# Performance work log

Hardware: AMD Instinct MI355X
Metric: run time of the kernel (lower is better)

Reference implementation:

```python
import jax, jax.numpy as jnp
import numpy as np

MIN_CONF = 0.1      # forward kwarg min_conf (also used as rasterize conf_thresh)
NMS_KS = 3
ITERS = 30
LAM = 0.8
LAMBDA_E = 2.0


def _resize_linear(x, out_size, axis):
    """1D linear resize along `axis` with align_corners=True semantics."""
    n = x.shape[axis]
    if out_size == n:
        return x
    if n == 1:
        reps = [1] * x.ndim
        reps[axis] = out_size
        return jnp.tile(x, reps)
    pos = jnp.arange(out_size, dtype=x.dtype) * ((n - 1) / (out_size - 1))
    lo = jnp.clip(jnp.floor(pos).astype(jnp.int32), 0, n - 1)
    hi = jnp.minimum(lo + 1, n - 1)
    w = pos - lo.astype(x.dtype)
    shp = [1] * x.ndim
    shp[axis] = out_size
    w = w.reshape(shp)
    xl = jnp.take(x, lo, axis=axis)
    xh = jnp.take(x, hi, axis=axis)
    return xl * (1.0 - w) + xh * w


def _interp3d_prob(P_lr, Dhr, H, W):
    """Trilinear (separable) upsample of [B,D,H4,W4] prob volume + renorm over D."""
    x = _resize_linear(P_lr, Dhr, 1)
    x = _resize_linear(x, H, 2)
    x = _resize_linear(x, W, 3)
    return x / (x.sum(1, keepdims=True) + 1e-6)


def _shift(x, dy, dx):
    """Replicate-padded spatial shift of [B,1,H,W] (matches torch _shift)."""
    H, W = x.shape[-2], x.shape[-1]
    p = jnp.pad(x, ((0, 0), (0, 0), (max(dy, 0), max(-dy, 0)), (max(dx, 0), max(-dx, 0))), mode='edge')
    return p[..., max(-dy, 0):H + max(-dy, 0), max(-dx, 0):W + max(-dx, 0)]


def _forward(P_lr, edge, occ, H, W, topk):
    B, Dlr, H4, W4 = P_lr.shape
    scale_x = float(W) / float(W4)
    Dhr = max(1, int(round(Dlr * scale_x)))

    # _fullres_prob is @torch.no_grad in the original -> stop_gradient
    P_full = jax.lax.stop_gradient(_interp3d_prob(P_lr, Dhr, H, W))  # [B,Dhr,H,W]

    d_vals = jnp.arange(Dhr, dtype=P_full.dtype)[None, :, None, None]
    disp_init = (P_full * d_vals).sum(1, keepdims=True)  # soft-argmin [B,1,H,W]

    # --- extract_sparse_anchors (dense, jit-friendly equivalent) ---
    pmax = P_full.max(1)                      # [B,H,W]
    d_hat = jnp.argmax(P_full, 1)             # [B,H,W]
    top2 = jax.lax.top_k(jnp.moveaxis(P_full, 1, -1), 2)[0]  # [B,H,W,2]
    p2 = top2[..., 1]
    psr = pmax / (p2 + 1e-6)
    conf = pmax * jnp.tanh(psr)
    conf = conf * jnp.exp(-2.0 * edge[:, 0]) * jnp.clip(1.0 - occ[:, 0], 0.0, None)

    # 2D NMS (ties kept): max_pool2d 3x3 stride 1, SAME padding with -inf
    pool = jax.lax.reduce_window(conf, -np.inf, jax.lax.max,
                                 (1, NMS_KS, NMS_KS), (1, 1, 1), 'SAME')
    keep = (conf >= MIN_CONF) & (conf >= pool)  # [B,H,W]

    # per-batch topk cap on anchors
    HW = H * W
    flat = jnp.where(keep, conf, -jnp.inf).reshape(B, HW)
    vals, idx = jax.lax.top_k(flat, topk)
    ok = vals > -jnp.inf
    def _scatter(i, v):
        return jnp.zeros((HW,), dtype=bool).at[i].set(v)
    keep_final = jax.vmap(_scatter)(idx, ok).reshape(B, H, W)[:, None]  # [B,1,H,W]

    # --- rasterize_dense_uspf ---
    d_map = jnp.where(keep_final, jnp.clip(d_hat, 0, Dhr - 1).astype(jnp.float32)[:, None], 0.0)
    c_map = jnp.where(keep_final, jnp.clip(conf, 0.0, 1.0)[:, None], 0.0)
    valid = keep_final & (c_map >= MIN_CONF)

    # --- refine_with_sparse_anchors_full: edge-aware diffusion of residual ---
    delta = jax.lax.stop_gradient(d_map - disp_init)
    m = jax.lax.stop_gradient(c_map * valid.astype(jnp.float32))

    e, o = edge, occ
    e_up, o_up = _shift(e, -1, 0), _shift(o, -1, 0)
    e_dn, o_dn = _shift(e, 1, 0), _shift(o, 1, 0)
    e_lf, o_lf = _shift(e, 0, -1), _shift(o, 0, -1)
    e_rt, o_rt = _shift(e, 0, 1), _shift(o, 0, 1)
    w_up = jnp.exp(-LAMBDA_E * (e + e_up) / 2) * (1 - o) * (1 - o_up)
    w_dn = jnp.exp(-LAMBDA_E * (e + e_dn) / 2) * (1 - o) * (1 - o_dn)
    w_lf = jnp.exp(-LAMBDA_E * (e + e_lf) / 2) * (1 - o) * (1 - o_lf)
    w_rt = jnp.exp(-LAMBDA_E * (e + e_rt) / 2) * (1 - o) * (1 - o_rt)
    w_sum = w_up + w_dn + w_lf + w_rt + 1e-6
    denom = m + LAM * w_sum + 1e-6
    num0 = m * delta

    def body(_, R):
        nbr = (w_up * _shift(R, -1, 0) + w_dn * _shift(R, 1, 0)
               + w_lf * _shift(R, 0, -1) + w_rt * _shift(R, 0, 1))
        return (num0 + LAM * nbr) / denom

    R = jax.lax.fori_loop(0, ITERS, body, jnp.zeros_like(disp_init))
    disp_full = jnp.clip(disp_init + R, 0.0, None)
    return disp_full


def setup_inputs() -> dict:
    key = jax.random.key(0)
    k1, k2, k3 = jax.random.split(key, 3)
    # spiky probability volume over D so that confident anchors exist
    P_lr = jax.nn.softmax(8.0 * jax.random.normal(k1, (1, 32, 96, 192), dtype=jnp.float32), axis=1)
    edge = 0.2 * jax.random.uniform(k2, (1, 1, 384, 768), dtype=jnp.float32)
    occ = 0.2 * jax.random.uniform(k3, (1, 1, 384, 768), dtype=jnp.float32)
    return {"P_lr": P_lr, "edge": edge, "occ": occ, "H": 384, "W": 768, "topk": 8000}


def reference(P_lr, edge, occ, H, W, topk):
    return _forward(P_lr, edge, occ, H, W, topk)
```

## Files before the change

### kernel.cpp

```cpp
#include <hip/hip_runtime.h>
#include <hip/hip_bf16.h>

typedef unsigned int u32;
typedef unsigned long long u64;

#define HH 384
#define WW 768
#define HW (HH*WW)
#define H4 96
#define W4 192
#define DLR 32
#define TOPK 8000
#define NTH 256
#define NBLK (HW/NTH)

#define PTW 18
#define PTH 3

#define JIW 48
#define JIH 32
#define JH  12
#define JRW 72
#define JRH 56
#define JNU (JRH*(JRW/4))
#define JGRID 192

#define KB16 0x3DCCu
#define NB16 448

struct SelState { u32 K, cutoff, idxcut; };

struct DTab {
    float A[32]; float B[32];
    int f[32]; int l[32];
    float w[128];
};
constexpr DTab mk_dtab(){
    DTab t{};
    const float CD = (float)(31.0/127.0);
    for (int k = 0; k < 32; ++k){ t.A[k]=0.f; t.B[k]=0.f; t.f[k]=-1; t.l[k]=-1; }
    for (int d = 0; d < 128; ++d){
        float pos = (float)d * CD;
        int lo = (int)pos; if (lo > 31) lo = 31;
        int hi = (lo+1 > 31) ? 31 : lo+1;
        float w = pos - (float)lo;
        t.w[d] = w;
        t.A[lo] += 1.0f - w;            t.A[hi] += w;
        t.B[lo] += (float)d*(1.0f - w); t.B[hi] += (float)d*w;
        if (t.f[lo] < 0) t.f[lo] = d;
        t.l[lo] = d;
    }
    return t;
}
static constexpr DTab DT = mk_dtab();

__global__ __launch_bounds__(NTH) void k_prob(const float* __restrict__ P,
        const float* __restrict__ edge, const float* __restrict__ occ,
        float* __restrict__ conf, float* __restrict__ disp0, u32* __restrict__ dhk,
        SelState* st){
    if (blockIdx.x == 0 && threadIdx.x == 0){
        st->K = 0; st->cutoff = 0; st->idxcut = 0x7FFFFFFFu;
    }

    __shared__ float Sl[DLR][PTH][PTW];
    __shared__ float YL[4][DLR][19];

    int bx = blockIdx.x % 12, by = blockIdx.x / 12;
    int X = bx*64, Y = by*4;
    const float CY = (float)(95.0/383.0);
    const float CX = (float)(191.0/767.0);

    float fy0 = (float)Y * CY; int y0min = (int)fy0; if (y0min > H4-1) y0min = H4-1;
    float fx0 = (float)X * CX; int x0min = (int)fx0; if (x0min > W4-1) x0min = W4-1;

    for (int e = threadIdx.x; e < DLR*PTH*PTW; e += NTH){
        int dl  = e / (PTH*PTW);
        int rem = e % (PTH*PTW);
        int ry  = rem / PTW;
        int cx  = rem % PTW;
        int gy = min(y0min + ry, H4-1);
        int gx = min(x0min + cx, W4-1);
        ((float*)Sl)[e] = P[dl*(H4*W4) + gy*W4 + gx];
    }
    __syncthreads();

    for (int e = threadIdx.x; e < 4*DLR*18; e += NTH){
        int ly  = e / (DLR*18);
        int rem = e % (DLR*18);
        int dl  = rem / 18;
        int cx  = rem % 18;
        float fy = (float)(Y + ly) * CY;
        int y0 = (int)fy; if (y0 > H4-1) y0 = H4-1;
        int y1 = min(y0+1, H4-1);
        float wy = fy - (float)y0;
        int ry = y0 - y0min, ryb = y1 - y0min;
        YL[ly][dl][cx] = Sl[dl][ry][cx]*(1.0f-wy) + Sl[dl][ryb][cx]*wy;
    }
    __syncthreads();

    int lx = threadIdx.x & 63, ly = threadIdx.x >> 6;
    int x = X + lx, y = Y + ly;
    int idx = y*WW + x;

    float fx = (float)x * CX;
    int x0 = (int)fx; if (x0 > W4-1) x0 = W4-1;
    float wx = fx - (float)x0;
    float omwx = 1.0f - wx;
    int cxl = x0 - x0min;

    float S[DLR];
    #pragma unroll
    for (int k = 0; k < DLR; ++k)
        S[k] = YL[ly][k][cxl]*omwx + YL[ly][k][cxl+1]*wx;

    float s0=0.f,s1=0.f,s2=0.f,s3=0.f, u0=0.f,u1=0.f,u2=0.f,u3=0.f;
    #pragma unroll
    for (int k = 0; k < DLR; k += 4){
        s0 = fmaf(DT.A[k  ], S[k  ], s0); u0 = fmaf(DT.B[k  ], S[k  ], u0);
        s1 = fmaf(DT.A[k+1], S[k+1], s1); u1 = fmaf(DT.B[k+1], S[k+1], u1);
        s2 = fmaf(DT.A[k+2], S[k+2], s2); u2 = fmaf(DT.B[k+2], S[k+2], u2);
        s3 = fmaf(DT.A[k+3], S[k+3], s3); u3 = fmaf(DT.B[k+3], S[k+3], u3);
    }
    float sum  = (s0+s1) + (s2+s3);
    float sumd = (u0+u1) + (u2+u3);

    float vmax = -1.f, v2 = -1.f; int dmax = 0;
    #pragma unroll
    for (int k = 0; k < 32; ++k){
        if (DT.f[k] < 0) continue;
        const int d0 = DT.f[k], d1 = DT.l[k];
        const int kh = (k+1 > 31) ? 31 : k+1;
        float Sk = S[k], Sh = S[kh];
        const float w0 = DT.w[d0], w1 = DT.w[d1];
        float vf = Sk*(1.0f-w0) + Sh*w0;
        float vl = Sk*(1.0f-w1) + Sh*w1;
        bool up = vl > vf;
        float segv = up ? vl : vf;
        int   segd = up ? d1 : d0;
        float vr = -1.f;
        if (d1 > d0){
            const float wa = DT.w[d1-1], wb = DT.w[d0+1];
            float va = Sk*(1.0f-wa) + Sh*wa;
            float vb = Sk*(1.0f-wb) + Sh*wb;
            vr = up ? va : vb;
        }
        if (segv > vmax){ v2 = fmaxf(vmax, vr); vmax = segv; dmax = segd; }
        else            { v2 = fmaxf(v2, segv); }
    }

    float inv  = 1.0f/(sum + 1e-6f);
    float pmax = vmax*inv, p2 = v2*inv;
    float psr  = pmax/(p2 + 1e-6f);
    float cf   = pmax * tanhf(psr);
    cf *= expf(-2.0f*edge[idx]) * fmaxf(1.0f - occ[idx], 0.0f);
    conf[idx]  = cf;
    disp0[idx] = sumd*inv;
    dhk[idx]   = (u32)dmax;
}

__global__ __launch_bounds__(NTH) void k_nms(const float* __restrict__ conf,
        const float* __restrict__ edge, const float* __restrict__ occ,
        u32* __restrict__ dhk, float4* __restrict__ w4raw,
        u64* __restrict__ list, SelState* st){
    __shared__ float Cs[6][66];
    __shared__ float Es[6][66];
    __shared__ float Os[6][66];
    int bx = blockIdx.x % 12, by = blockIdx.x / 12;
    int X = bx*64, Y = by*4;
    for (int e = threadIdx.x; e < 6*66; e += NTH){
        int ry = e / 66, cx = e % 66;
        int gy = Y + ry - 1, gx = X + cx - 1;
        bool in = ((u32)gy < (u32)HH) && ((u32)gx < (u32)WW);
        int cg = min(max(gy,0),HH-1)*WW + min(max(gx,0),WW-1);
        Cs[ry][cx] = in ? conf[cg] : -INFINITY;
        Es[ry][cx] = edge[cg];
        Os[ry][cx] = occ[cg];
    }
    __syncthreads();

    int lx = threadIdx.x & 63, ly = threadIdx.x >> 6;
    int x = X + lx, y = Y + ly;
    int idx = y*WW + x;

    float c = Cs[ly+1][lx+1];
    float pool = Cs[ly][lx];
    pool = fmaxf(pool, Cs[ly  ][lx+1]); pool = fmaxf(pool, Cs[ly  ][lx+2]);
    pool = fmaxf(pool, Cs[ly+1][lx  ]); pool = fmaxf(pool, Cs[ly+1][lx+1]);
    pool = fmaxf(pool, Cs[ly+1][lx+2]);
    pool = fmaxf(pool, Cs[ly+2][lx  ]); pool = fmaxf(pool, Cs[ly+2][lx+1]);
    pool = fmaxf(pool, Cs[ly+2][lx+2]);
    bool keep = (c >= 0.1f) && (c >= pool);
    dhk[idx] |= keep ? 256u : 0u;

    float e  = Es[ly+1][lx+1], o  = Os[ly+1][lx+1];
    float e1 = Es[ly+2][lx+1], o1 = Os[ly+2][lx+1];
    float e2 = Es[ly  ][lx+1], o2 = Os[ly  ][lx+1];
    float e3 = Es[ly+1][lx+2], o3 = Os[ly+1][lx+2];
    float e4 = Es[ly+1][lx  ], o4 = Os[ly+1][lx  ];
    float4 wp;
    wp.x = expf(-(e+e1))*(1.f-o)*(1.f-o1);
    wp.y = expf(-(e+e2))*(1.f-o)*(1.f-o2);
    wp.z = expf(-(e+e3))*(1.f-o)*(1.f-o3);
    wp.w = expf(-(e+e4))*(1.f-o)*(1.f-o4);
    w4raw[idx] = wp;

    u64 m = __ballot(keep);
    int lane = threadIdx.x & 63, wid = threadIdx.x >> 6;
    __shared__ u32 wc[4];
    __shared__ u32 wpre[4];
    __shared__ u32 bb;
    if (lane == 0) wc[wid] = (u32)__popcll(m);
    __syncthreads();
    if (threadIdx.x == 0){
        u32 s = 0;
        #pragma unroll
        for (int w = 0; w < 4; ++w){ wpre[w] = s; s += wc[w]; }
        bb = atomicAdd(&st->K, s);
    }
    __syncthreads();
    if (keep){
        u32 before = (u32)__popcll(m & ((1ull << lane) - 1ull));
        u32 pos = bb + wpre[wid] + before;
        list[pos] = ((u64)__float_as_uint(c) << 32) | (u32)idx;
    }
}

__global__ __launch_bounds__(1024) void k_sel(const u64* __restrict__ list,
        u64* __restrict__ side, SelState* st){
    u32 n = st->K;
    if (n <= TOPK) return;

    __shared__ u32 wh[16][NB16+1];
    __shared__ u32 hs[512];
    __shared__ u32 sc[512];
    __shared__ u32 hh[256];
    __shared__ u32 bc[3];
    __shared__ u32 snc;
    int t = threadIdx.x;
    int lane = t & 63, wv = t >> 6;

    for (int e = t; e < 16*(NB16+1); e += 1024) ((u32*)wh)[e] = 0;
    if (t == 0) snc = 0;
    __syncthreads();

    u32 nh = n >> 1;
    const ulonglong2* list2 = (const ulonglong2*)list;
    for (u32 p = t; p < nh; p += 1024){
        ulonglong2 e2 = list2[p];
        int b0 = (int)((u32)(e2.x >> 48)) - (int)KB16;
        int b1 = (int)((u32)(e2.y >> 48)) - (int)KB16;
        b0 = min(max(b0, 0), NB16-1);
        b1 = min(max(b1, 0), NB16-1);
        atomicAdd(&wh[wv][b0], 1u);
        atomicAdd(&wh[wv][b1], 1u);
    }
    if ((n & 1u) && t == 0){
        int b = (int)((u32)(list[n-1] >> 48)) - (int)KB16;
        b = min(max(b, 0), NB16-1);
        atomicAdd(&wh[0][b], 1u);
    }
    __syncthreads();
    if (t < 512){
        u32 s = 0;
        if (t < NB16){
            #pragma unroll
            for (int w = 0; w < 16; ++w) s += wh[w][t];
        }
        hs[t] = s;
    }
    __syncthreads();

    u32 rem = TOPK;
    if (t < 512) sc[t] = hs[511 - t];
    __syncthreads();
    for (int off = 1; off < 512; off <<= 1){
        u32 add = (t < 512 && t >= off) ? sc[t - off] : 0;
        __syncthreads();
        if (t < 512) sc[t] += add;
        __syncthreads();
    }
    if (t < 512){
        u32 Sd  = sc[511 - t];
        u32 Sd1 = (t == 511) ? 0u : sc[511 - (t+1)];
        if (Sd >= rem && Sd1 < rem){ bc[0] = (u32)t; bc[1] = rem - Sd1; }
    }
    __syncthreads();
    u32 p16 = KB16 + bc[0];
    rem = bc[1];
    __syncthreads();

    if (t < 256) hh[t] = 0;
    __syncthreads();
    u32 npad = (n + 1023u) & ~1023u;
    for (u32 i = t; i < npad; i += 1024){
        bool match = false; u64 e = 0; u32 key = 0;
        if (i < n){
            e = list[i];
            key = (u32)(e >> 32);
            match = (key >> 16) == p16;
        }
        u64 mb = __ballot(match);
        u32 cnt = (u32)__popcll(mb);
        if (cnt){
            int ldr = (int)(__ffsll((long long)mb) - 1);
            u32 base = 0;
            if (lane == ldr) base = atomicAdd(&snc, cnt);
            base = __shfl(base, ldr);
            if (match){
                u32 before = (u32)__popcll(mb & ((1ull << lane) - 1ull));
                side[base + before] = e;
                atomicAdd(&hh[(key >> 8) & 255u], 1u);
            }
        }
    }
    __syncthreads();
    u32 msz = snc;

    if (t < 256) sc[t] = hh[255 - t];
    __syncthreads();
    for (int off = 1; off < 256; off <<= 1){
        u32 add = (t < 256 && t >= off) ? sc[t - off] : 0;
        __syncthreads();
        if (t < 256) sc[t] += add;
        __syncthreads();
    }
    if (t < 256){
        u32 Sd  = sc[255 - t];
        u32 Sd1 = (t == 255) ? 0u : sc[255 - (t+1)];
        if (Sd >= rem && Sd1 < rem){ bc[0] = (u32)t; bc[1] = rem - Sd1; }
    }
    __syncthreads();
    u32 d1 = bc[0]; rem = bc[1];
    u32 pref24 = (p16 << 8) | d1;
    __syncthreads();

    if (t < 256) hh[t] = 0;
    __syncthreads();
    u32 mpad = (msz + 1023u) & ~1023u;
    for (u32 i = t; i < mpad; i += 1024){
        if (i < msz){
            u32 key = (u32)(side[i] >> 32);
            if ((key >> 8) == pref24) atomicAdd(&hh[key & 255u], 1u);
        }
    }
    __syncthreads();
    if (t < 256) sc[t] = hh[255 - t];
    __syncthreads();
    for (int off = 1; off < 256; off <<= 1){
        u32 add = (t < 256 && t >= off) ? sc[t - off] : 0;
        __syncthreads();
        if (t < 256) sc[t] += add;
        __syncthreads();
    }
    if (t < 256){
        u32 Sd  = sc[255 - t];
        u32 Sd1 = (t == 255) ? 0u : sc[255 - (t+1)];
        if (Sd >= rem && Sd1 < rem){ bc[0] = (u32)t; bc[1] = rem - Sd1; bc[2] = hh[t]; }
    }
    __syncthreads();
    u32 cutoff = (pref24 << 8) | bc[0];
    rem = bc[1];
    u32 tie_h = bc[2];
    __syncthreads();

    u32 idxcut = 0x7FFFFFFFu;
    if (rem != tie_h){
        u32 iprefix = 0, irem = rem;
        for (int b = 2; b >= 0; --b){
            if (t < 256) hh[t] = 0;
            __syncthreads();
            int shift = 8*b;
            for (u32 i = t; i < mpad; i += 1024){
                if (i < msz){
                    u64 e = side[i];
                    u32 key = (u32)(e >> 32);
                    u32 idx = (u32)e;
                    if (key == cutoff && (((u64)(idx ^ iprefix)) >> (shift+8)) == 0)
                        atomicAdd(&hh[(idx >> shift) & 255u], 1u);
                }
            }
            __syncthreads();
            if (t < 256) sc[t] = hh[t];
            __syncthreads();
            for (int off = 1; off < 256; off <<= 1){
                u32 add = (t < 256 && t >= off) ? sc[t - off] : 0;
                __syncthreads();
                if (t < 256) sc[t] += add;
                __syncthreads();
            }
            if (t < 256){
                u32 Pd = sc[t];
                u32 Pm = (t == 0) ? 0u : sc[t-1];
                if (Pd >= irem && Pm < irem){ bc[0] = (u32)t; bc[1] = irem - Pm; }
            }
            __syncthreads();
            iprefix |= bc[0] << shift; irem = bc[1];
            __syncthreads();
        }
        idxcut = iprefix;
    }
    if (t == 0){ st->cutoff = cutoff; st->idxcut = idxcut; }
}

template<int FUSED, int FINAL>
__global__ __launch_bounds__(NTH) void k_jacT(
        const float* __restrict__ Rin, float* __restrict__ Rout,
        const float4* __restrict__ Wp, const float* __restrict__ Nh,
        float4* __restrict__ Ws, float* __restrict__ Nho,
        const float* __restrict__ conf, const float* __restrict__ disp0,
        const u32* __restrict__ dhk, const SelState* __restrict__ st,
        float* __restrict__ out, int K){
    __shared__ float Rs[2][JRH*JRW];
    int tid = threadIdx.x;
    int bx = blockIdx.x & 15, by = blockIdx.x >> 4;
    int ry0 = by*JIH - JH, cx0 = bx*JIW - JH;

    float4 Wt[4][4];
    float4 Nt[4];
    float4 Ct[4];

    u32 cut = 0, idxcut = 0;
    if (FUSED){ cut = st->cutoff; idxcut = st->idxcut; }

    #pragma unroll
    for (int k = 0; k < 4; ++k){
        int u = tid + k*NTH;
        if (u < JNU){
            int r = u / 18, c = (u % 18) << 2;
            int gy = ry0 + r;
            int cgy = min(max(gy,0),HH-1);
            float4 n4, r4;
            #pragma unroll
            for (int j = 0; j < 4; ++j){
                int gx = cx0 + c + j;
                int cgx = min(max(gx,0),WW-1);
                int g = cgy*WW + cgx;
                if (FUSED){
                    u32 dv = dhk[g];
                    float cf = conf[g];
                    u32 key = __float_as_uint(cf);
                    bool kf = (dv & 256u) &&
                              (key > cut || (key == cut && (u32)g <= idxcut));
                    float mm = kf ? fminf(fmaxf(cf, 0.0f), 1.0f) : 0.0f;
                    float4 wr = Wp[g];
                    float wsum = wr.x + wr.y + wr.z + wr.w + 1e-6f;
                    float den = mm + 0.8f*wsum + 1e-6f;
                    float n0 = mm * ((float)(dv & 255u) - disp0[g]);
                    float nh = n0 / den;
                    float sc = 0.8f / den;
                    wr.x *= sc; wr.y *= sc; wr.z *= sc; wr.w *= sc;
                    Wt[k][j] = wr;
                    ((float*)&n4)[j] = nh;
                    ((float*)&r4)[j] = nh;
                } else {
                    Wt[k][j] = Wp[g];
                    ((float*)&n4)[j] = Nh[g];
                    ((float*)&r4)[j] = Rin[g];
                }
            }
            Nt[k] = n4; Ct[k] = r4;
            *(float4*)&Rs[0][r*JRW + c] = r4;
            if (FUSED){
                if (r >= JH && r < JH+JIH && c >= JH && c < JH+JIW){
                    int g2 = (ry0 + r)*WW + (cx0 + c);
                    #pragma unroll
                    for (int j = 0; j < 4; ++j) Ws[g2 + j] = Wt[k][j];
                    *(float4*)&Nho[g2] = n4;
                }
            }
        }
    }
    __syncthreads();

    int cur = 0;
    for (int ts = 1; ts <= K; ++ts){
        #pragma unroll
        for (int k = 0; k < 4; ++k){
            int u = tid + k*NTH;
            if (u < JNU){
                int r = u / 18, c = (u % 18) << 2;
                int gy = ry0 + r;
                float4 C = Ct[k];
                int rm = (r > 0) ? r-1 : r;
                int rp = (r < JRH-1) ? r+1 : r;
                float4 up = *(const float4*)&Rs[cur][rm*JRW + c];
                float4 dn = *(const float4*)&Rs[cur][rp*JRW + c];
                if (gy == 0)    up = C;
                if (gy == HH-1) dn = C;
                float xl = Rs[cur][r*JRW + ((c > 0) ? c-1 : c)];
                float xr = Rs[cur][r*JRW + ((c+4 < JRW) ? c+4 : JRW-1)];
                int gx0 = cx0 + c;
                if (gx0 == 0)        xl = C.x;
                if (gx0 + 3 == WW-1) xr = C.w;
                float4 nv;
                nv.x = Nt[k].x + Wt[k][0].x*up.x + Wt[k][0].y*dn.x + Wt[k][0].z*xl  + Wt[k][0].w*C.y;
                nv.y = Nt[k].y + Wt[k][1].x*up.y + Wt[k][1].y*dn.y + Wt[k][1].z*C.x + Wt[k][1].w*C.z;
                nv.z = Nt[k].z + Wt[k][2].x*up.z + Wt[k][2].y*dn.z + Wt[k][2].z*C.y + Wt[k][2].w*C.w;
                nv.w = Nt[k].w + Wt[k][3].x*up.w + Wt[k][3].y*dn.w + Wt[k][3].z*C.z + Wt[k][3].w*xr;
                bool rowin = (r >= ts) && (r < JRH - ts);
                int cl = ts, ch = JRW - ts;
                nv.x = (rowin && c   >= cl && c   < ch) ? nv.x : C.x;
                nv.y = (rowin && c+1 >= cl && c+1 < ch) ? nv.y : C.y;
                nv.z = (rowin && c+2 >= cl && c+2 < ch) ? nv.z : C.z;
                nv.w = (rowin && c+3 >= cl && c+3 < ch) ? nv.w : C.w;
                *(float4*)&Rs[cur^1][r*JRW + c] = nv;
                Ct[k] = nv;
            }
        }
        __syncthreads();
        cur ^= 1;
    }

    #pragma unroll
    for (int k = 0; k < 4; ++k){
        int u = tid + k*NTH;
        if (u < JNU){
            int r = u / 18, c = (u % 18) << 2;
            if (r >= JH && r < JH+JIH && c >= JH && c < JH+JIW){
                int g = (ry0 + r)*WW + (cx0 + c);
                if (FINAL){
                    float4 d0 = *(const float4*)&disp0[g];
                    float4 o;
                    o.x = fmaxf(d0.x + Ct[k].x, 0.0f);
                    o.y = fmaxf(d0.y + Ct[k].y, 0.0f);
                    o.z = fmaxf(d0.z + Ct[k].z, 0.0f);
                    o.w = fmaxf(d0.w + Ct[k].w, 0.0f);
                    *(float4*)&out[g] = o;
                } else {
                    *(float4*)&Rout[g] = Ct[k];
                }
            }
        }
    }
}

extern "C" void kernel_launch(void* const* d_in, const int* in_sizes, int n_in,
                              void* d_out, int out_size, void* d_ws, size_t ws_size,
                              hipStream_t stream) {
    const float* P    = (const float*)d_in[0];
    const float* edge = (const float*)d_in[1];
    const float* occ  = (const float*)d_in[2];
    float* out = (float*)d_out;

    float*  conf   = (float*)d_ws;
    float*  disp0  = conf + HW;
    float*  nhat   = disp0 + HW;
    float*  Ra     = nhat + HW;
    float*  Rb     = Ra + HW;
    u32*    dhk    = (u32*)(Rb + HW);
    float4* w4raw  = (float4*)(dhk + HW);
    float4* w4s    = w4raw + HW;
    u64*    list   = (u64*)(w4s + HW);
    u64*    side   = list + HW;
    SelState* st   = (SelState*)(side + HW);

    dim3 grid(NBLK), block(NTH);
    k_prob<<<grid, block, 0, stream>>>(P, edge, occ, conf, disp0, dhk, st);
    k_nms<<<grid, block, 0, stream>>>(conf, edge, occ, dhk, w4raw, list, st);
    k_sel<<<1, 1024, 0, stream>>>(list, side, st);

    dim3 jgrid(JGRID);
    k_jacT<1,0><<<jgrid, block, 0, stream>>>(nullptr, Ra, w4raw, nullptr, w4s, nhat,
                                             conf, disp0, dhk, st, out, 10);
    k_jacT<0,0><<<jgrid, block, 0, stream>>>(Ra, Rb, w4s, nhat, nullptr, nullptr,
                                             conf, disp0, dhk, st, out, 10);
    k_jacT<0,1><<<jgrid, block, 0, stream>>>(Rb, nullptr, w4s, nhat, nullptr, nullptr,
                                             conf, disp0, dhk, st, out, 9);
}
```

Before: 105.8 us.

## Fuse prob and NMS kernels, use per-block anchor slots, deepen Jacobi halo

```diff
diff --git a/kernel.cpp b/kernel.cpp
--- a/kernel.cpp
+++ b/kernel.cpp
@@ -14,21 +14,26 @@
 #define NTH 256
 #define NBLK (HW/NTH)
 
-#define PTW 18
-#define PTH 3
+#define CNB 66
+#define CNR 6
+#define PTW 19
+#define PTH 4
 
 #define JIW 48
 #define JIH 32
-#define JH  12
-#define JRW 72
-#define JRH 56
-#define JNU (JRH*(JRW/4))
+#define JH  16
+#define JRW 80
+#define JRH 64
+#define JUPR (JRW/4)
+#define JNU (JRH*JUPR)
+#define JNTH 512
 #define JGRID 192
 
 #define KB16 0x3DCCu
 #define NB16 448
-
-struct SelState { u32 K, cutoff, idxcut; };
+#define NSLOT (NBLK*256)
+
+struct SelState { u32 cutoff, idxcut; };
 
 struct DTab {
     float A[32]; float B[32];
@@ -54,24 +59,26 @@
 }
 static constexpr DTab DT = mk_dtab();
 
-__global__ __launch_bounds__(NTH) void k_prob(const float* __restrict__ P,
+__global__ __launch_bounds__(NTH) void k_pn(const float* __restrict__ P,
         const float* __restrict__ edge, const float* __restrict__ occ,
         float* __restrict__ conf, float* __restrict__ disp0, u32* __restrict__ dhk,
-        SelState* st){
-    if (blockIdx.x == 0 && threadIdx.x == 0){
-        st->K = 0; st->cutoff = 0; st->idxcut = 0x7FFFFFFFu;
-    }
-
+        float4* __restrict__ w4raw, u64* __restrict__ list, u32* __restrict__ blk_cnt){
     __shared__ float Sl[DLR][PTH][PTW];
-    __shared__ float YL[4][DLR][19];
+    __shared__ float YL[CNR][DLR][20];
+    __shared__ float Es[CNR][CNB];
+    __shared__ float Os[CNR][CNB];
+    __shared__ float Cs[CNR][CNB];
+    __shared__ u32   Ds[CNR][CNB];
 
     int bx = blockIdx.x % 12, by = blockIdx.x / 12;
     int X = bx*64, Y = by*4;
     const float CY = (float)(95.0/383.0);
     const float CX = (float)(191.0/767.0);
 
-    float fy0 = (float)Y * CY; int y0min = (int)fy0; if (y0min > H4-1) y0min = H4-1;
-    float fx0 = (float)X * CX; int x0min = (int)fx0; if (x0min > W4-1) x0min = W4-1;
+    int yb = (Y > 0) ? (Y-1) : 0;
+    int xb = (X > 0) ? (X-1) : 0;
+    int y0min = (int)((float)yb * CY); if (y0min > H4-1) y0min = H4-1;
+    int x0min = (int)((float)xb * CX); if (x0min > W4-1) x0min = W4-1;
 
     for (int e = threadIdx.x; e < DLR*PTH*PTW; e += NTH){
         int dl  = e / (PTH*PTW);
@@ -82,99 +89,95 @@
         int gx = min(x0min + cx, W4-1);
         ((float*)Sl)[e] = P[dl*(H4*W4) + gy*W4 + gx];
     }
-    __syncthreads();
-
-    for (int e = threadIdx.x; e < 4*DLR*18; e += NTH){
-        int ly  = e / (DLR*18);
-        int rem = e % (DLR*18);
-        int dl  = rem / 18;
-        int cx  = rem % 18;
-        float fy = (float)(Y + ly) * CY;
+    for (int e = threadIdx.x; e < CNR*CNB; e += NTH){
+        int ry = e / CNB, cx = e % CNB;
+        int gy = min(max(Y + ry - 1, 0), HH-1);
+        int gx = min(max(X + cx - 1, 0), WW-1);
+        int cg = gy*WW + gx;
+        Es[ry][cx] = edge[cg];
+        Os[ry][cx] = occ[cg];
+    }
+    __syncthreads();
+
+    for (int e = threadIdx.x; e < CNR*DLR*PTW; e += NTH){
+        int row = e / (DLR*PTW);
+        int rem = e % (DLR*PTW);
+        int dl  = rem / PTW;
+        int cx  = rem % PTW;
+        int gyo = min(max(Y + row - 1, 0), HH-1);
+        float fy = (float)gyo * CY;
         int y0 = (int)fy; if (y0 > H4-1) y0 = H4-1;
         int y1 = min(y0+1, H4-1);
         float wy = fy - (float)y0;
         int ry = y0 - y0min, ryb = y1 - y0min;
-        YL[ly][dl][cx] = Sl[dl][ry][cx]*(1.0f-wy) + Sl[dl][ryb][cx]*wy;
-    }
-    __syncthreads();
-
-    int lx = threadIdx.x & 63, ly = threadIdx.x >> 6;
-    int x = X + lx, y = Y + ly;
-    int idx = y*WW + x;
-
-    float fx = (float)x * CX;
-    int x0 = (int)fx; if (x0 > W4-1) x0 = W4-1;
-    float wx = fx - (float)x0;
-    float omwx = 1.0f - wx;
-    int cxl = x0 - x0min;
-
-    float S[DLR];
-    #pragma unroll
-    for (int k = 0; k < DLR; ++k)
-        S[k] = YL[ly][k][cxl]*omwx + YL[ly][k][cxl+1]*wx;
-
-    float s0=0.f,s1=0.f,s2=0.f,s3=0.f, u0=0.f,u1=0.f,u2=0.f,u3=0.f;
-    #pragma unroll
-    for (int k = 0; k < DLR; k += 4){
-        s0 = fmaf(DT.A[k  ], S[k  ], s0); u0 = fmaf(DT.B[k  ], S[k  ], u0);
-        s1 = fmaf(DT.A[k+1], S[k+1], s1); u1 = fmaf(DT.B[k+1], S[k+1], u1);
-        s2 = fmaf(DT.A[k+2], S[k+2], s2); u2 = fmaf(DT.B[k+2], S[k+2], u2);
-        s3 = fmaf(DT.A[k+3], S[k+3], s3); u3 = fmaf(DT.B[k+3], S[k+3], u3);
-    }
-    float sum  = (s0+s1) + (s2+s3);
-    float sumd = (u0+u1) + (u2+u3);
-
-    float vmax = -1.f, v2 = -1.f; int dmax = 0;
-    #pragma unroll
-    for (int k = 0; k < 32; ++k){
-        if (DT.f[k] < 0) continue;
-        const int d0 = DT.f[k], d1 = DT.l[k];
-        const int kh = (k+1 > 31) ? 31 : k+1;
-        float Sk = S[k], Sh = S[kh];
-        const float w0 = DT.w[d0], w1 = DT.w[d1];
-        float vf = Sk*(1.0f-w0) + Sh*w0;
-        float vl = Sk*(1.0f-w1) + Sh*w1;
-        bool up = vl > vf;
-        float segv = up ? vl : vf;
-        int   segd = up ? d1 : d0;
-        float vr = -1.f;
-        if (d1 > d0){
-            const float wa = DT.w[d1-1], wb = DT.w[d0+1];
-            float va = Sk*(1.0f-wa) + Sh*wa;
-            float vb = Sk*(1.0f-wb) + Sh*wb;
-            vr = up ? va : vb;
-        }
-        if (segv > vmax){ v2 = fmaxf(vmax, vr); vmax = segv; dmax = segd; }
-        else            { v2 = fmaxf(v2, segv); }
-    }
-
-    float inv  = 1.0f/(sum + 1e-6f);
-    float pmax = vmax*inv, p2 = v2*inv;
-    float psr  = pmax/(p2 + 1e-6f);
-    float cf   = pmax * tanhf(psr);
-    cf *= expf(-2.0f*edge[idx]) * fmaxf(1.0f - occ[idx], 0.0f);
-    conf[idx]  = cf;
-    disp0[idx] = sumd*inv;
-    dhk[idx]   = (u32)dmax;
-}
-
-__global__ __launch_bounds__(NTH) void k_nms(const float* __restrict__ conf,
-        const float* __restrict__ edge, const float* __restrict__ occ,
-        u32* __restrict__ dhk, float4* __restrict__ w4raw,
-        u64* __restrict__ list, SelState* st){
-    __shared__ float Cs[6][66];
-    __shared__ float Es[6][66];
-    __shared__ float Os[6][66];
-    int bx = blockIdx.x % 12, by = blockIdx.x / 12;
-    int X = bx*64, Y = by*4;
-    for (int e = threadIdx.x; e < 6*66; e += NTH){
-        int ry = e / 66, cx = e % 66;
+        YL[row][dl][cx] = Sl[dl][ry][cx]*(1.0f-wy) + Sl[dl][ryb][cx]*wy;
+    }
+    __syncthreads();
+
+    for (int e = threadIdx.x; e < CNR*CNB; e += NTH){
+        int ry = e / CNB, cx = e % CNB;
         int gy = Y + ry - 1, gx = X + cx - 1;
         bool in = ((u32)gy < (u32)HH) && ((u32)gx < (u32)WW);
-        int cg = min(max(gy,0),HH-1)*WW + min(max(gx,0),WW-1);
-        Cs[ry][cx] = in ? conf[cg] : -INFINITY;
-        Es[ry][cx] = edge[cg];
-        Os[ry][cx] = occ[cg];
+        if (!in){ Cs[ry][cx] = -INFINITY; continue; }
+
+        float fx = (float)gx * CX;
+        int x0 = (int)fx; if (x0 > W4-1) x0 = W4-1;
+        float wx = fx - (float)x0;
+        float omwx = 1.0f - wx;
+        int cxl = x0 - x0min;
+
+        float S[DLR];
+        #pragma unroll
+        for (int k = 0; k < DLR; ++k)
+            S[k] = YL[ry][k][cxl]*omwx + YL[ry][k][cxl+1]*wx;
+
+        float s0=0.f,s1=0.f,s2=0.f,s3=0.f, u0=0.f,u1=0.f,u2=0.f,u3=0.f;
+        #pragma unroll
+        for (int k = 0; k < DLR; k += 4){
+            s0 = fmaf(DT.A[k  ], S[k  ], s0); u0 = fmaf(DT.B[k  ], S[k  ], u0);
+            s1 = fmaf(DT.A[k+1], S[k+1], s1); u1 = fmaf(DT.B[k+1], S[k+1], u1);
+            s2 = fmaf(DT.A[k+2], S[k+2], s2); u2 = fmaf(DT.B[k+2], S[k+2], u2);
+            s3 = fmaf(DT.A[k+3], S[k+3], s3); u3 = fmaf(DT.B[k+3], S[k+3], u3);
+        }
+        float sum  = (s0+s1) + (s2+s3);
+        float sumd = (u0+u1) + (u2+u3);
+
+        float vmax = -1.f, v2 = -1.f; int dmax = 0;
+        #pragma unroll
+        for (int k = 0; k < 32; ++k){
+            if (DT.f[k] < 0) continue;
+            const int d0 = DT.f[k], d1 = DT.l[k];
+            const int kh = (k+1 > 31) ? 31 : k+1;
+            float Sk = S[k], Sh = S[kh];
+            const float w0 = DT.w[d0], w1 = DT.w[d1];
+            float vf = Sk*(1.0f-w0) + Sh*w0;
+            float vl = Sk*(1.0f-w1) + Sh*w1;
+            bool up = vl > vf;
+            float segv = up ? vl : vf;
+            int   segd = up ? d1 : d0;
+            float vr = -1.f;
+            if (d1 > d0){
+                const float wa = DT.w[d1-1], wb = DT.w[d0+1];
+                float va = Sk*(1.0f-wa) + Sh*wa;
+                float vb = Sk*(1.0f-wb) + Sh*wb;
+                vr = up ? va : vb;
+            }
+            if (segv > vmax){ v2 = fmaxf(vmax, vr); vmax = segv; dmax = segd; }
+            else            { v2 = fmaxf(v2, segv); }
+        }
+
+        float inv  = 1.0f/(sum + 1e-6f);
+        float pmax = vmax*inv, p2 = v2*inv;
+        float psr  = pmax/(p2 + 1e-6f);
+        float cf   = pmax * tanhf(psr);
+        cf *= expf(-2.0f*Es[ry][cx]) * fmaxf(1.0f - Os[ry][cx], 0.0f);
+        Cs[ry][cx] = cf;
+        if (ry >= 1 && ry <= 4 && cx >= 1 && cx <= 64){
+            int g = gy*WW + gx;
+            conf[g]  = cf;
+            disp0[g] = sumd*inv;
+            Ds[ry][cx] = (u32)dmax;
+        }
     }
     __syncthreads();
 
@@ -190,7 +193,7 @@
     pool = fmaxf(pool, Cs[ly+2][lx  ]); pool = fmaxf(pool, Cs[ly+2][lx+1]);
     pool = fmaxf(pool, Cs[ly+2][lx+2]);
     bool keep = (c >= 0.1f) && (c >= pool);
-    dhk[idx] |= keep ? 256u : 0u;
+    dhk[idx] = Ds[ly+1][lx+1] | (keep ? 256u : 0u);
 
     float e  = Es[ly+1][lx+1], o  = Os[ly+1][lx+1];
     float e1 = Es[ly+2][lx+1], o1 = Os[ly+2][lx+1];
@@ -208,70 +211,72 @@
     int lane = threadIdx.x & 63, wid = threadIdx.x >> 6;
     __shared__ u32 wc[4];
     __shared__ u32 wpre[4];
-    __shared__ u32 bb;
     if (lane == 0) wc[wid] = (u32)__popcll(m);
     __syncthreads();
     if (threadIdx.x == 0){
         u32 s = 0;
         #pragma unroll
         for (int w = 0; w < 4; ++w){ wpre[w] = s; s += wc[w]; }
-        bb = atomicAdd(&st->K, s);
+        blk_cnt[blockIdx.x] = s;
     }
     __syncthreads();
     if (keep){
         u32 before = (u32)__popcll(m & ((1ull << lane) - 1ull));
-        u32 pos = bb + wpre[wid] + before;
-        list[pos] = ((u64)__float_as_uint(c) << 32) | (u32)idx;
+        list[blockIdx.x*256u + wpre[wid] + before] =
+            ((u64)__float_as_uint(c) << 32) | (u32)idx;
     }
 }
 
 __global__ __launch_bounds__(1024) void k_sel(const u64* __restrict__ list,
-        u64* __restrict__ side, SelState* st){
-    u32 n = st->K;
-    if (n <= TOPK) return;
-
+        const u32* __restrict__ blk_cnt, u64* __restrict__ side, SelState* st){
+    __shared__ u32 cnt_s[NBLK];
     __shared__ u32 wh[16][NB16+1];
-    __shared__ u32 hs[512];
     __shared__ u32 sc[512];
     __shared__ u32 hh[256];
     __shared__ u32 bc[3];
-    __shared__ u32 snc;
+    __shared__ u32 snn, snc;
     int t = threadIdx.x;
-    int lane = t & 63, wv = t >> 6;
-
+    int lane = t & 63;
+
+    if (t == 0){ snn = 0; snc = 0; }
     for (int e = t; e < 16*(NB16+1); e += 1024) ((u32*)wh)[e] = 0;
-    if (t == 0) snc = 0;
-    __syncthreads();
-
-    u32 nh = n >> 1;
-    const ulonglong2* list2 = (const ulonglong2*)list;
-    for (u32 p = t; p < nh; p += 1024){
-        ulonglong2 e2 = list2[p];
-        int b0 = (int)((u32)(e2.x >> 48)) - (int)KB16;
-        int b1 = (int)((u32)(e2.y >> 48)) - (int)KB16;
-        b0 = min(max(b0, 0), NB16-1);
-        b1 = min(max(b1, 0), NB16-1);
-        atomicAdd(&wh[wv][b0], 1u);
-        atomicAdd(&wh[wv][b1], 1u);
-    }
-    if ((n & 1u) && t == 0){
-        int b = (int)((u32)(list[n-1] >> 48)) - (int)KB16;
-        b = min(max(b, 0), NB16-1);
-        atomicAdd(&wh[0][b], 1u);
-    }
-    __syncthreads();
+    u32 myc = 0;
+    if (t < NBLK){ u32 v = blk_cnt[t]; cnt_s[t] = v; myc = v; }
+    if (t + 1024 < NBLK){ u32 v = blk_cnt[t+1024]; cnt_s[t+1024] = v; myc += v; }
+    __syncthreads();
+    #pragma unroll
+    for (int o = 32; o > 0; o >>= 1) myc += __shfl_down(myc, o);
+    if (lane == 0 && myc) atomicAdd(&snn, myc);
+    __syncthreads();
+    u32 n = snn;
+    if (n <= TOPK){
+        if (t == 0){ st->cutoff = 0; st->idxcut = 0x7FFFFFFFu; }
+        return;
+    }
+    int wv = t >> 6;
+
+    const u32* hi32 = (const u32*)list;
+    for (u32 i = t; i < NSLOT; i += 1024){
+        u32 ch = i >> 8;
+        if ((i & 255u) < cnt_s[ch]){
+            u32 key = hi32[2*i+1];
+            int b = (int)(key >> 16) - (int)KB16;
+            b = min(max(b, 0), NB16-1);
+            atomicAdd(&wh[wv][b], 1u);
+        }
+    }
+    __syncthreads();
+
+    u32 rem = TOPK;
     if (t < 512){
         u32 s = 0;
-        if (t < NB16){
+        int d = 511 - t;
+        if (d < NB16){
             #pragma unroll
-            for (int w = 0; w < 16; ++w) s += wh[w][t];
-        }
-        hs[t] = s;
-    }
-    __syncthreads();
-
-    u32 rem = TOPK;
-    if (t < 512) sc[t] = hs[511 - t];
+            for (int w = 0; w < 16; ++w) s += wh[w][d];
+        }
+        sc[t] = s;
+    }
     __syncthreads();
     for (int off = 1; off < 512; off <<= 1){
         u32 add = (t < 512 && t >= off) ? sc[t - off] : 0;
@@ -291,10 +296,10 @@
 
     if (t < 256) hh[t] = 0;
     __syncthreads();
-    u32 npad = (n + 1023u) & ~1023u;
-    for (u32 i = t; i < npad; i += 1024){
+    for (u32 i = t; i < NSLOT; i += 1024){
+        u32 ch = i >> 8;
         bool match = false; u64 e = 0; u32 key = 0;
-        if (i < n){
+        if ((i & 255u) < cnt_s[ch]){
             e = list[i];
             key = (u32)(e >> 32);
             match = (key >> 16) == p16;
@@ -330,8 +335,8 @@
         if (Sd >= rem && Sd1 < rem){ bc[0] = (u32)t; bc[1] = rem - Sd1; }
     }
     __syncthreads();
-    u32 d1 = bc[0]; rem = bc[1];
-    u32 pref24 = (p16 << 8) | d1;
+    u32 pref24 = (p16 << 8) | bc[0];
+    rem = bc[1];
     __syncthreads();
 
     if (t < 256) hh[t] = 0;
@@ -403,7 +408,7 @@
 }
 
 template<int FUSED, int FINAL>
-__global__ __launch_bounds__(NTH) void k_jacT(
+__global__ __launch_bounds__(JNTH) void k_jacT(
         const float* __restrict__ Rin, float* __restrict__ Rout,
         const float4* __restrict__ Wp, const float* __restrict__ Nh,
         float4* __restrict__ Ws, float* __restrict__ Nho,
@@ -415,18 +420,18 @@
     int bx = blockIdx.x & 15, by = blockIdx.x >> 4;
     int ry0 = by*JIH - JH, cx0 = bx*JIW - JH;
 
-    float4 Wt[4][4];
-    float4 Nt[4];
-    float4 Ct[4];
+    float4 Wt[3][4];
+    float4 Nt[3];
+    float4 Ct[3];
 
     u32 cut = 0, idxcut = 0;
     if (FUSED){ cut = st->cutoff; idxcut = st->idxcut; }
 
     #pragma unroll
-    for (int k = 0; k < 4; ++k){
-        int u = tid + k*NTH;
+    for (int k = 0; k < 3; ++k){
+        int u = tid + k*JNTH;
         if (u < JNU){
-            int r = u / 18, c = (u % 18) << 2;
+            int r = u / JUPR, c = (u % JUPR) << 2;
             int gy = ry0 + r;
             int cgy = min(max(gy,0),HH-1);
             float4 n4, r4;
@@ -475,10 +480,10 @@
     int cur = 0;
     for (int ts = 1; ts <= K; ++ts){
         #pragma unroll
-        for (int k = 0; k < 4; ++k){
-            int u = tid + k*NTH;
+        for (int k = 0; k < 3; ++k){
+            int u = tid + k*JNTH;
             if (u < JNU){
-                int r = u / 18, c = (u % 18) << 2;
+                int r = u / JUPR, c = (u % JUPR) << 2;
                 int gy = ry0 + r;
                 float4 C = Ct[k];
                 int rm = (r > 0) ? r-1 : r;
@@ -512,10 +517,10 @@
     }
 
     #pragma unroll
-    for (int k = 0; k < 4; ++k){
-        int u = tid + k*NTH;
+    for (int k = 0; k < 3; ++k){
+        int u = tid + k*JNTH;
         if (u < JNU){
-            int r = u / 18, c = (u % 18) << 2;
+            int r = u / JUPR, c = (u % JUPR) << 2;
             if (r >= JH && r < JH+JIH && c >= JH && c < JH+JIW){
                 int g = (ry0 + r)*WW + (cx0 + c);
                 if (FINAL){
@@ -546,24 +551,21 @@
     float*  disp0  = conf + HW;
     float*  nhat   = disp0 + HW;
     float*  Ra     = nhat + HW;
-    float*  Rb     = Ra + HW;
-    u32*    dhk    = (u32*)(Rb + HW);
+    u32*    dhk    = (u32*)(Ra + HW);
     float4* w4raw  = (float4*)(dhk + HW);
     float4* w4s    = w4raw + HW;
     u64*    list   = (u64*)(w4s + HW);
-    u64*    side   = list + HW;
-    SelState* st   = (SelState*)(side + HW);
-
-    dim3 grid(NBLK), block(NTH);
-    k_prob<<<grid, block, 0, stream>>>(P, edge, occ, conf, disp0, dhk, st);
-    k_nms<<<grid, block, 0, stream>>>(conf, edge, occ, dhk, w4raw, list, st);
-    k_sel<<<1, 1024, 0, stream>>>(list, side, st);
-
-    dim3 jgrid(JGRID);
-    k_jacT<1,0><<<jgrid, block, 0, stream>>>(nullptr, Ra, w4raw, nullptr, w4s, nhat,
-                                             conf, disp0, dhk, st, out, 10);
-    k_jacT<0,0><<<jgrid, block, 0, stream>>>(Ra, Rb, w4s, nhat, nullptr, nullptr,
-                                             conf, disp0, dhk, st, out, 10);
-    k_jacT<0,1><<<jgrid, block, 0, stream>>>(Rb, nullptr, w4s, nhat, nullptr, nullptr,
-                                             conf, disp0, dhk, st, out, 9);
+    u64*    side   = list + NSLOT;
+    u32*    blk_cnt= (u32*)(side + NSLOT);
+    SelState* st   = (SelState*)(blk_cnt + NBLK);
+
+    k_pn<<<dim3(NBLK), dim3(NTH), 0, stream>>>(P, edge, occ, conf, disp0, dhk,
+                                               w4raw, list, blk_cnt);
+    k_sel<<<1, 1024, 0, stream>>>(list, blk_cnt, side, st);
+
+    dim3 jgrid(JGRID), jblock(JNTH);
+    k_jacT<1,0><<<jgrid, jblock, 0, stream>>>(nullptr, Ra, w4raw, nullptr, w4s, nhat,
+                                              conf, disp0, dhk, st, out, 15);
+    k_jacT<0,1><<<jgrid, jblock, 0, stream>>>(Ra, nullptr, w4s, nhat, nullptr, nullptr,
+                                              conf, disp0, dhk, st, out, 14);
 }
```

New measurement: 231.3 us. +118.7%, slower.
